# Kernel tuning notes

Measured on AMD Instinct MI355X. Metric: run time of the kernel, lower is better.

## Reference

```python
import jax, jax.numpy as jnp
import numpy as np

B, L, H = 256, 2048, 64

def _min_gru(x, Wz, bz, Wh, bh):
    # x: [B, L, Din] -> h: [B, L, H] via parallel scan of h_t = (1-z_t)*h_{t-1} + z_t*h~_t, h_0 = 0
    z = jax.nn.sigmoid(jnp.einsum('bli,ih->blh', x, Wz) + bz)
    h_tilde = jnp.einsum('bli,ih->blh', x, Wh) + bh
    a = 1.0 - z
    b = z * h_tilde
    def combine(c1, c2):
        a1, b1 = c1
        a2, b2 = c2
        return a1 * a2, b1 * a2 + b2
    _, h = jax.lax.associative_scan(combine, (a, b), axis=1)
    return h

def _stacked(x, Wz0, bz0, Wh0, bh0, Wz1, bz1, Wh1, bh1, Wo, bo):
    h = _min_gru(x, Wz0, bz0, Wh0, bh0)
    h = _min_gru(h, Wz1, bz1, Wh1, bh1)
    return jnp.einsum('blh,ho->blo', h, Wo) + bo  # [B, L, 1]

def setup_inputs():
    key = jax.random.key(0)
    ks = jax.random.split(key, 32)
    inputs = jax.random.bernoulli(ks[0], 0.5, (B, L)).astype(jnp.float32)
    p_array = jax.random.permutation(ks[1], L).astype(jnp.int32)
    def lin(k, fin, fout):
        return (jax.random.normal(k, (fin, fout), jnp.float32) / np.float32(np.sqrt(fin)))
    d = {'inputs': inputs, 'p_array': p_array}
    i = 2
    for r in (1, 2):
        for nm, fin, fout in (('z0', 1, H), ('h0', 1, H), ('z1', H, H), ('h1', H, H), ('o', H, 1)):
            d['w%d%s' % (r, nm)] = lin(ks[i], fin, fout); i += 1
            d['b%d%s' % (r, nm)] = jnp.zeros((fout,), jnp.float32)
    return d

def reference(inputs, p_array, w1z0, b1z0, w1h0, b1h0, w1z1, b1z1, w1h1, b1h1, w1o, b1o,
              w2z0, b2z0, w2h0, b2h0, w2z1, b2z1, w2h1, b2h1, w2o, b2o):
    x = inputs[..., None]                      # [B, L, 1]
    x_sys = _stacked(x, w1z0, b1z0, w1h0, b1h0, w1z1, b1z1, w1h1, b1h1, w1o, b1o)
    x_int = x[:, p_array, :]                   # interleave along sequence dim
    x_p1 = _stacked(x_int, w2z0, b2z0, w2h0, b2h0, w2z1, b2z1, w2h1, b2h1, w2o, b2o)
    x_tx = jnp.concatenate([x_sys, x_p1], axis=2)  # [B, L, 2]
    mean = jnp.mean(x_tx)
    std = jnp.std(x_tx, ddof=1)                # torch.std is unbiased by default
    return (x_tx - mean) / std                 # squeeze(dim=2) is a no-op on size-2 dim
```

## Files before the change

kernel.cpp:

```cpp
#include <hip/hip_runtime.h>

#define BB 256
#define LL 2048
#define HH 64
#define TT 64
#define SS 68
#define NCH (LL / TT)
#define NTOT (BB * LL * 2)

typedef __attribute__((ext_vector_type(8))) short bf16x8;
typedef __attribute__((ext_vector_type(4))) float f32x4;

__device__ __forceinline__ float rcp_(float x)  { return __builtin_amdgcn_rcpf(x); }

__device__ __forceinline__ short f2bf_rne(float f) {
    union { float f; unsigned u; } v; v.f = f;
    unsigned r = v.u + 0x7fff + ((v.u >> 16) & 1);
    return (short)(r >> 16);
}

__device__ __forceinline__ unsigned perm_hi16(float f_hi, float f_lo) {
    union { float f; unsigned u; } a, b;
    a.f = f_hi; b.f = f_lo;
    return __builtin_amdgcn_perm(a.u, b.u, 0x07060302u);
}

template<int D>
__device__ __forceinline__ float rshr(float x) {
    union { float f; int i; } u, r;
    u.f = x;
    r.i = __builtin_amdgcn_update_dpp(0, u.i, 0x110 | D, 0xF, 0xF, true);
    return r.f;
}

__device__ __forceinline__ float bcast7(float x) {
    union { float f; int i; } u, r;
    u.f = x;
    r.i = __builtin_amdgcn_ds_swizzle(u.i, 0x00F8);
    return r.f;
}

__device__ __forceinline__ void p1_scan(const unsigned* __restrict__ bw, int c,
                                        float a0v, float b0v, float a1v, float b1v,
                                        int seg, int col0,
                                        float& carry, float* sh)
{
    const unsigned bits = (bw[c * 2 + (seg >> 2)] >> ((seg & 3) << 3)) & 0xffu;
    float A = 1.0f, Bv = 0.0f;
    #pragma unroll
    for (int i = 0; i < 8; ++i) {
        const bool on = (bits >> i) & 1u;
        const float a = on ? a1v : a0v;
        const float b = on ? b1v : b0v;
        A  = A * a;
        Bv = fmaf(Bv, a, b);
    }
    {
        const float Au = rshr<1>(A), Bu = rshr<1>(Bv);
        if (seg >= 1) { const float Ac = A; A = Au * Ac; Bv = fmaf(Bu, Ac, Bv); }
    }
    {
        const float Au = rshr<2>(A), Bu = rshr<2>(Bv);
        if (seg >= 2) { const float Ac = A; A = Au * Ac; Bv = fmaf(Bu, Ac, Bv); }
    }
    {
        const float Au = rshr<4>(A), Bu = rshr<4>(Bv);
        if (seg >= 4) { const float Ac = A; A = Au * Ac; Bv = fmaf(Bu, Ac, Bv); }
    }
    float Ae = rshr<1>(A), Be = rshr<1>(Bv);
    if (seg == 0) { Ae = 1.0f; Be = 0.0f; }
    float cc = fmaf(Ae, carry, Be);
    #pragma unroll
    for (int i = 0; i < 8; ++i) {
        const bool on = (bits >> i) & 1u;
        const float a = on ? a1v : a0v;
        const float b = on ? b1v : b0v;
        cc = fmaf(a, cc, b);
        sh[(seg * 8 + i) * SS + col0] = cc;
    }
    carry = bcast7(cc);
}

__global__ void __launch_bounds__(512)
__attribute__((amdgpu_waves_per_eu(4, 4)))
gru_fused(const float* __restrict__ x, const int* __restrict__ p,
               const float* __restrict__ w1z0, const float* __restrict__ b1z0,
               const float* __restrict__ w1h0, const float* __restrict__ b1h0,
               const float* __restrict__ w1z1, const float* __restrict__ b1z1,
               const float* __restrict__ w1h1, const float* __restrict__ b1h1,
               const float* __restrict__ w1o,  const float* __restrict__ b1o,
               const float* __restrict__ w2z0, const float* __restrict__ b2z0,
               const float* __restrict__ w2h0, const float* __restrict__ b2h0,
               const float* __restrict__ w2z1, const float* __restrict__ b2z1,
               const float* __restrict__ w2h1, const float* __restrict__ b2h1,
               const float* __restrict__ w2o,  const float* __restrict__ b2o,
               float* __restrict__ out, float* __restrict__ ws)
{
    const int  b  = blockIdx.x;
    const bool pm = (blockIdx.y != 0);

    const float* wz0 = pm ? w2z0 : w1z0;
    const float* bz0 = pm ? b2z0 : b1z0;
    const float* wh0 = pm ? w2h0 : w1h0;
    const float* bh0 = pm ? b2h0 : b1h0;
    const float* wz1 = pm ? w2z1 : w1z1;
    const float* bz1 = pm ? b2z1 : b1z1;
    const float* wh1 = pm ? w2h1 : w1h1;
    const float* bh1 = pm ? b2h1 : b1h1;
    const float* wo  = pm ? w2o  : w1o;
    const float* bov = pm ? b2o  : b1o;

    const int tid   = threadIdx.x;
    const int lane  = tid & 63;
    const int tg    = tid >> 6;
    const int tgu   = __builtin_amdgcn_readfirstlane(tg);
    const int twu   = tgu & 3;
    const int hwu   = tgu >> 2;
    const int q     = lane >> 4;
    const int n     = lane & 15;
    const int seg   = lane & 7;
    const int hidx  = (tgu << 3) | (lane >> 3);

    __shared__ __align__(16) float s_h[2 * TT * SS];
    __shared__ unsigned long long s_xb[LL / 64];
    __shared__ float2 s_w[2][2][4][32];
    __shared__ float s_o[2][4][16];
    __shared__ float s_red[16];

    const float* xrow = x + (size_t)b * LL;

    #pragma unroll
    for (int g = 0; g < 4; ++g) {
        const int idx = g * 512 + tid;
        const int src = pm ? p[idx] : idx;
        const unsigned long long m = __ballot(xrow[src] != 0.0f);
        if (lane == 0) s_xb[g * 8 + tgu] = m;
    }
    const unsigned* bw = (const unsigned*)s_xb;

    const float z0v = rcp_(1.0f + __expf(-bz0[hidx]));
    const float z1v = rcp_(1.0f + __expf(-(wz0[hidx] + bz0[hidx])));
    const float a0v = 1.0f - z0v, b0v = z0v * bh0[hidx];
    const float a1v = 1.0f - z1v, b1v = z1v * (wh0[hidx] + bh0[hidx]);

    float rbz1[2], rbh1[2], rwo4[2];
    #pragma unroll
    for (int ht = 0; ht < 2; ++ht) {
        const int h = hwu * 32 + ht * 16 + n;
        rbz1[ht] = bz1[h];
        rbh1[ht] = bh1[h];
        rwo4[ht] = wo[h];
    }
    const float bo = bov[0];

    bf16x8 wfz[2][2], wfh[2][2];
    for (int ks = 0; ks < 2; ++ks) {
        for (int ht = 0; ht < 2; ++ht) {
            #pragma unroll
            for (int j = 0; j < 8; ++j) {
                const int kk = ks * 32 + q * 8 + j;
                const int h  = hwu * 32 + ht * 16 + n;
                wfz[ks][ht][j] = f2bf_rne(wz1[kk * HH + h]);
                wfh[ks][ht][j] = f2bf_rne(wh1[kk * HH + h]);
            }
        }
    }

    float carry0 = 0.0f;
    float carry1[2] = {0.0f, 0.0f};
    f32x4 ga[2], gb[2];
    float Aqe[2], Bqe[2];
    float pvo[4] = {0, 0, 0, 0};
    float lsum = 0.0f, lsum2 = 0.0f;
    float* outp = out + (pm ? 1 : 0);
    const int t0 = twu * 16;
    const int col0 = hidx ^ (seg << 2);
    const int sswz = (twu * 2 + (n >> 3)) << 2;

    auto g2_step = [&](int cm) {
        if (cm > 0 && hwu == 0 && n == 15) {
            #pragma unroll
            for (int r = 0; r < 4; ++r) {
                const float v = pvo[r] + s_o[(cm - 1) & 1][twu][q * 4 + r] + bo;
                outp[((size_t)b * LL + (cm - 1) * TT + t0 + q * 4 + r) * 2] = v;
                lsum += v;
                lsum2 = fmaf(v, v, lsum2);
            }
        }
        const int buf = cm & 1;
        float Acm[2] = {1, 1}, Bcm[2] = {0, 0};
        float Ap[2], Bp[2];
        #pragma unroll
        for (int w = 0; w < 4; ++w) {
            #pragma unroll
            for (int ht = 0; ht < 2; ++ht) {
                if (w == twu) { Ap[ht] = Acm[ht]; Bp[ht] = Bcm[ht]; }
                const float2 ab = s_w[buf][hwu][w][ht * 16 + n];
                Bcm[ht] = fmaf(ab.x, Bcm[ht], ab.y);
                Acm[ht] *= ab.x;
            }
        }
        float vo[4] = {0, 0, 0, 0};
        #pragma unroll
        for (int ht = 0; ht < 2; ++ht) {
            float cc = fmaf(Aqe[ht], fmaf(Ap[ht], carry1[ht], Bp[ht]), Bqe[ht]);
            #pragma unroll
            for (int r = 0; r < 4; ++r) {
                cc = fmaf(ga[ht][r], cc, gb[ht][r]);
                vo[r] = fmaf(cc, rwo4[ht], vo[r]);
            }
            carry1[ht] = fmaf(Acm[ht], carry1[ht], Bcm[ht]);
        }
        #pragma unroll
        for (int r = 0; r < 4; ++r) {
            vo[r] += rshr<1>(vo[r]);
            vo[r] += rshr<2>(vo[r]);
            vo[r] += rshr<4>(vo[r]);
            vo[r] += rshr<8>(vo[r]);
        }
        if (n == 15) {
            if (hwu) {
                #pragma unroll
                for (int r = 0; r < 4; ++r) s_o[buf][twu][q * 4 + r] = vo[r];
            } else {
                #pragma unroll
                for (int r = 0; r < 4; ++r) pvo[r] = vo[r];
            }
        }
    };

    __syncthreads();

    p1_scan(bw, 0, a0v, b0v, a1v, b1v, seg, col0, carry0, s_h);
    __syncthreads();

    for (int c = 0; c < NCH; ++c) {
        const int cp1 = c + 1;

        if (c > 0) g2_step(c - 1);

        {
            #pragma unroll
            for (int ht = 0; ht < 2; ++ht) {
                ga[ht] = (f32x4){rbz1[ht], rbz1[ht], rbz1[ht], rbz1[ht]};
                gb[ht] = (f32x4){rbh1[ht], rbh1[ht], rbh1[ht], rbh1[ht]};
            }
            const float* shR = s_h + (c & 1) * (TT * SS);
            #pragma unroll
            for (int ks = 0; ks < 2; ++ks) {
                const int base = ks * 32 + q * 8;
                const float* rowp = &shR[(t0 + n) * SS];
                const float4 av0 = *(const float4*)(rowp + (base ^ sswz));
                const float4 av1 = *(const float4*)(rowp + ((base + 4) ^ sswz));
                float af[8] = {av0.x, av0.y, av0.z, av0.w, av1.x, av1.y, av1.z, av1.w};
                union { bf16x8 v; unsigned d[4]; } ahi, alo;
                float rem[8];
                #pragma unroll
                for (int j = 0; j < 8; ++j) {
                    union { float f; unsigned u; } uf; uf.f = af[j];
                    union { unsigned u; float f; } hf; hf.u = uf.u & 0xffff0000u;
                    rem[j] = af[j] - hf.f;
                }
                #pragma unroll
                for (int k = 0; k < 4; ++k) {
                    ahi.d[k] = perm_hi16(af[2 * k + 1], af[2 * k]);
                    alo.d[k] = perm_hi16(rem[2 * k + 1], rem[2 * k]);
                }
                #pragma unroll
                for (int ht = 0; ht < 2; ++ht) {
                    ga[ht] = __builtin_amdgcn_mfma_f32_16x16x32_bf16(ahi.v, wfz[ks][ht], ga[ht], 0, 0, 0);
                    ga[ht] = __builtin_amdgcn_mfma_f32_16x16x32_bf16(alo.v, wfz[ks][ht], ga[ht], 0, 0, 0);
                    gb[ht] = __builtin_amdgcn_mfma_f32_16x16x32_bf16(ahi.v, wfh[ks][ht], gb[ht], 0, 0, 0);
                    gb[ht] = __builtin_amdgcn_mfma_f32_16x16x32_bf16(alo.v, wfh[ks][ht], gb[ht], 0, 0, 0);
                }
            }
            #pragma unroll
            for (int ht = 0; ht < 2; ++ht) {
                #pragma unroll
                for (int r = 0; r < 4; ++r) {
                    const float v   = ga[ht][r];
                    const float a   = rcp_(1.0f + __expf(v));
                    const float htl = gb[ht][r];
                    ga[ht][r] = a;
                    gb[ht][r] = fmaf(-a, htl, htl);
                }
            }
            float Aq[2], Bq[2];
            #pragma unroll
            for (int ht = 0; ht < 2; ++ht) {
                float A = 1.0f, B = 0.0f;
                #pragma unroll
                for (int r = 0; r < 4; ++r) {
                    B = fmaf(ga[ht][r], B, gb[ht][r]);
                    A = A * ga[ht][r];
                }
                Aq[ht] = A; Bq[ht] = B;
            }
            #pragma unroll
            for (int ht = 0; ht < 2; ++ht) {
                const float Au = __shfl_up(Aq[ht], 16), Bu = __shfl_up(Bq[ht], 16);
                if (q >= 1) { const float Ac = Aq[ht]; Aq[ht] = Ac * Au; Bq[ht] = fmaf(Ac, Bu, Bq[ht]); }
            }
            #pragma unroll
            for (int ht = 0; ht < 2; ++ht) {
                const float Au = __shfl_up(Aq[ht], 32), Bu = __shfl_up(Bq[ht], 32);
                if (q >= 2) { const float Ac = Aq[ht]; Aq[ht] = Ac * Au; Bq[ht] = fmaf(Ac, Bu, Bq[ht]); }
            }
            #pragma unroll
            for (int ht = 0; ht < 2; ++ht) {
                const float Ae = __shfl_up(Aq[ht], 16), Be = __shfl_up(Bq[ht], 16);
                Aqe[ht] = (q == 0) ? 1.0f : Ae;
                Bqe[ht] = (q == 0) ? 0.0f : Be;
            }
            if (q == 3) {
                #pragma unroll
                for (int ht = 0; ht < 2; ++ht)
                    s_w[c & 1][hwu][twu][ht * 16 + n] = make_float2(Aq[ht], Bq[ht]);
            }
        }

        if (cp1 < NCH)
            p1_scan(bw, cp1, a0v, b0v, a1v, b1v, seg, col0, carry0,
                    s_h + (cp1 & 1) * (TT * SS));

        __syncthreads();
    }

    g2_step(NCH - 1);
    __syncthreads();
    if (hwu == 0 && n == 15) {
        #pragma unroll
        for (int r = 0; r < 4; ++r) {
            const float v = pvo[r] + s_o[(NCH - 1) & 1][twu][q * 4 + r] + bo;
            outp[((size_t)b * LL + (NCH - 1) * TT + t0 + q * 4 + r) * 2] = v;
            lsum += v;
            lsum2 = fmaf(v, v, lsum2);
        }
    }

    #pragma unroll
    for (int o = 32; o; o >>= 1) {
        lsum  += __shfl_down(lsum, o);
        lsum2 += __shfl_down(lsum2, o);
    }
    if (lane == 0) { s_red[tgu] = lsum; s_red[8 + tgu] = lsum2; }
    __syncthreads();
    if (tid == 0) {
        float s = 0.0f, s2 = 0.0f;
        #pragma unroll
        for (int i = 0; i < 8; ++i) { s += s_red[i]; s2 += s_red[8 + i]; }
        const int gb2 = b * 2 + (pm ? 1 : 0);
        ws[2 * gb2]     = s;
        ws[2 * gb2 + 1] = s2;
    }
}

__global__ void normalize_k(float* __restrict__ out, const float* __restrict__ ws)
{
    __shared__ float s_red[8];
    float s = 0.0f, s2 = 0.0f;
    for (int i = threadIdx.x; i < 2 * BB; i += 256) {
        s  += ws[2 * i];
        s2 += ws[2 * i + 1];
    }
    #pragma unroll
    for (int o = 32; o; o >>= 1) {
        s  += __shfl_down(s, o);
        s2 += __shfl_down(s2, o);
    }
    const int wid = threadIdx.x >> 6;
    if ((threadIdx.x & 63) == 0) { s_red[wid] = s; s_red[4 + wid] = s2; }
    __syncthreads();
    const float tot  = s_red[0] + s_red[1] + s_red[2] + s_red[3];
    const float tot2 = s_red[4] + s_red[5] + s_red[6] + s_red[7];
    const float N    = (float)NTOT;
    const float mean = tot / N;
    const float var  = (tot2 - N * mean * mean) / (N - 1.0f);
    const float inv  = rsqrtf(var);

    const int i = blockIdx.x * blockDim.x + threadIdx.x;
    float4* o4 = (float4*)out;
    float4 v = o4[i];
    v.x = (v.x - mean) * inv;
    v.y = (v.y - mean) * inv;
    v.z = (v.z - mean) * inv;
    v.w = (v.w - mean) * inv;
    o4[i] = v;
}

extern "C" void kernel_launch(void* const* d_in, const int* in_sizes, int n_in,
                              void* d_out, int out_size, void* d_ws, size_t ws_size,
                              hipStream_t stream)
{
    (void)in_sizes; (void)n_in; (void)out_size; (void)ws_size;
    const float* x = (const float*)d_in[0];
    const int*   p = (const int*)d_in[1];
    float* out = (float*)d_out;
    float* ws  = (float*)d_ws;

    dim3 grid(BB, 2);
    gru_fused<<<grid, 512, 0, stream>>>(
        x, p,
        (const float*)d_in[2],  (const float*)d_in[3],
        (const float*)d_in[4],  (const float*)d_in[5],
        (const float*)d_in[6],  (const float*)d_in[7],
        (const float*)d_in[8],  (const float*)d_in[9],
        (const float*)d_in[10], (const float*)d_in[11],
        (const float*)d_in[12], (const float*)d_in[13],
        (const float*)d_in[14], (const float*)d_in[15],
        (const float*)d_in[16], (const float*)d_in[17],
        (const float*)d_in[18], (const float*)d_in[19],
        (const float*)d_in[20], (const float*)d_in[21],
        out, ws);

    normalize_k<<<NTOT / 4 / 256, 256, 0, stream>>>(out, ws);
}
```

Measured before the change: 185.5 us.

## Double threads per block and store layer-1 states pre-split into bf16 hi/lo

```diff
diff --git a/kernel.cpp b/kernel.cpp
--- a/kernel.cpp
+++ b/kernel.cpp
@@ -4,7 +4,7 @@
 #define LL 2048
 #define HH 64
 #define TT 64
-#define SS 68
+#define SH 72
 #define NCH (LL / TT)
 #define NTOT (BB * LL * 2)
 
@@ -17,12 +17,6 @@
     union { float f; unsigned u; } v; v.f = f;
     unsigned r = v.u + 0x7fff + ((v.u >> 16) & 1);
     return (short)(r >> 16);
-}
-
-__device__ __forceinline__ unsigned perm_hi16(float f_hi, float f_lo) {
-    union { float f; unsigned u; } a, b;
-    a.f = f_hi; b.f = f_lo;
-    return __builtin_amdgcn_perm(a.u, b.u, 0x07060302u);
 }
 
 template<int D>
@@ -33,27 +27,27 @@
     return r.f;
 }
 
-__device__ __forceinline__ float bcast7(float x) {
+__device__ __forceinline__ float bcast15(float x) {
     union { float f; int i; } u, r;
     u.f = x;
-    r.i = __builtin_amdgcn_ds_swizzle(u.i, 0x00F8);
+    r.i = __builtin_amdgcn_ds_swizzle(u.i, 0x01F0);
     return r.f;
 }
 
 __device__ __forceinline__ void p1_scan(const unsigned* __restrict__ bw, int c,
                                         float a0v, float b0v, float a1v, float b1v,
-                                        int seg, int col0,
-                                        float& carry, float* sh)
+                                        int seg, int pos0,
+                                        float& carry, short* shh, short* shl)
 {
-    const unsigned bits = (bw[c * 2 + (seg >> 2)] >> ((seg & 3) << 3)) & 0xffu;
+    const unsigned bits = (bw[c * 2 + (seg >> 3)] >> ((seg & 7) << 2)) & 0xFu;
     float A = 1.0f, Bv = 0.0f;
     #pragma unroll
-    for (int i = 0; i < 8; ++i) {
+    for (int i = 0; i < 4; ++i) {
         const bool on = (bits >> i) & 1u;
         const float a = on ? a1v : a0v;
-        const float b = on ? b1v : b0v;
+        const float bb = on ? b1v : b0v;
         A  = A * a;
-        Bv = fmaf(Bv, a, b);
+        Bv = fmaf(Bv, a, bb);
     }
     {
         const float Au = rshr<1>(A), Bu = rshr<1>(Bv);
@@ -67,22 +61,31 @@
         const float Au = rshr<4>(A), Bu = rshr<4>(Bv);
         if (seg >= 4) { const float Ac = A; A = Au * Ac; Bv = fmaf(Bu, Ac, Bv); }
     }
+    {
+        const float Au = rshr<8>(A), Bu = rshr<8>(Bv);
+        if (seg >= 8) { const float Ac = A; A = Au * Ac; Bv = fmaf(Bu, Ac, Bv); }
+    }
     float Ae = rshr<1>(A), Be = rshr<1>(Bv);
     if (seg == 0) { Ae = 1.0f; Be = 0.0f; }
     float cc = fmaf(Ae, carry, Be);
     #pragma unroll
-    for (int i = 0; i < 8; ++i) {
+    for (int i = 0; i < 4; ++i) {
         const bool on = (bits >> i) & 1u;
         const float a = on ? a1v : a0v;
-        const float b = on ? b1v : b0v;
-        cc = fmaf(a, cc, b);
-        sh[(seg * 8 + i) * SS + col0] = cc;
-    }
-    carry = bcast7(cc);
-}
-
-__global__ void __launch_bounds__(512)
-__attribute__((amdgpu_waves_per_eu(4, 4)))
+        const float bb = on ? b1v : b0v;
+        cc = fmaf(a, cc, bb);
+        const int row = seg * 4 + i;
+        union { float f; unsigned u; } uf; uf.f = cc;
+        shh[row * SH + pos0] = (short)(uf.u >> 16);
+        union { unsigned u; float f; } hf; hf.u = uf.u & 0xffff0000u;
+        union { float f; unsigned u; } ur; ur.f = cc - hf.f;
+        shl[row * SH + pos0] = (short)(ur.u >> 16);
+    }
+    carry = bcast15(cc);
+}
+
+__global__ void __launch_bounds__(1024)
+__attribute__((amdgpu_waves_per_eu(8, 8)))
 gru_fused(const float* __restrict__ x, const int* __restrict__ p,
                const float* __restrict__ w1z0, const float* __restrict__ b1z0,
                const float* __restrict__ w1h0, const float* __restrict__ b1h0,
@@ -118,23 +121,24 @@
     const int hwu   = tgu >> 2;
     const int q     = lane >> 4;
     const int n     = lane & 15;
-    const int seg   = lane & 7;
-    const int hidx  = (tgu << 3) | (lane >> 3);
-
-    __shared__ __align__(16) float s_h[2 * TT * SS];
+    const int seg   = lane & 15;
+    const int hidx  = (tgu << 2) | (lane >> 4);
+
     __shared__ unsigned long long s_xb[LL / 64];
-    __shared__ float2 s_w[2][2][4][32];
-    __shared__ float s_o[2][4][16];
-    __shared__ float s_red[16];
+    __shared__ __align__(16) short s_hh[2][TT][SH];
+    __shared__ __align__(16) short s_hl[2][TT][SH];
+    __shared__ float2 s_w[2][4][4][16];
+    __shared__ float  s_o[2][3][4][16];
+    __shared__ float  s_red[32];
 
     const float* xrow = x + (size_t)b * LL;
 
     #pragma unroll
-    for (int g = 0; g < 4; ++g) {
-        const int idx = g * 512 + tid;
+    for (int g = 0; g < 2; ++g) {
+        const int idx = g * 1024 + tid;
         const int src = pm ? p[idx] : idx;
         const unsigned long long m = __ballot(xrow[src] != 0.0f);
-        if (lane == 0) s_xb[g * 8 + tgu] = m;
+        if (lane == 0) s_xb[g * 16 + tgu] = m;
     }
     const unsigned* bw = (const unsigned*)s_xb;
 
@@ -143,73 +147,65 @@
     const float a0v = 1.0f - z0v, b0v = z0v * bh0[hidx];
     const float a1v = 1.0f - z1v, b1v = z1v * (wh0[hidx] + bh0[hidx]);
 
-    float rbz1[2], rbh1[2], rwo4[2];
-    #pragma unroll
-    for (int ht = 0; ht < 2; ++ht) {
-        const int h = hwu * 32 + ht * 16 + n;
-        rbz1[ht] = bz1[h];
-        rbh1[ht] = bh1[h];
-        rwo4[ht] = wo[h];
-    }
-    const float bo = bov[0];
-
-    bf16x8 wfz[2][2], wfh[2][2];
+    const int hq = hwu * 16 + n;
+    const float rbz1 = bz1[hq];
+    const float rbh1 = bh1[hq];
+    const float rwo  = wo[hq];
+    const float bo   = bov[0];
+
+    bf16x8 wfz[2], wfh[2];
     for (int ks = 0; ks < 2; ++ks) {
-        for (int ht = 0; ht < 2; ++ht) {
-            #pragma unroll
-            for (int j = 0; j < 8; ++j) {
-                const int kk = ks * 32 + q * 8 + j;
-                const int h  = hwu * 32 + ht * 16 + n;
-                wfz[ks][ht][j] = f2bf_rne(wz1[kk * HH + h]);
-                wfh[ks][ht][j] = f2bf_rne(wh1[kk * HH + h]);
-            }
+        #pragma unroll
+        for (int j = 0; j < 8; ++j) {
+            const int kk = ks * 32 + q * 8 + j;
+            wfz[ks][j] = f2bf_rne(wz1[kk * HH + hq]);
+            wfh[ks][j] = f2bf_rne(wh1[kk * HH + hq]);
         }
     }
 
     float carry0 = 0.0f;
-    float carry1[2] = {0.0f, 0.0f};
-    f32x4 ga[2], gb[2];
-    float Aqe[2], Bqe[2];
+    float carry1 = 0.0f;
+    f32x4 ga, gb;
+    float Aqe, Bqe;
     float pvo[4] = {0, 0, 0, 0};
     float lsum = 0.0f, lsum2 = 0.0f;
     float* outp = out + (pm ? 1 : 0);
     const int t0 = twu * 16;
-    const int col0 = hidx ^ (seg << 2);
-    const int sswz = (twu * 2 + (n >> 3)) << 2;
+    const int pos0 = hidx ^ ((seg & 7) << 3);
+    const int sw   = ((twu * 4 + (n >> 2)) & 7) << 3;
 
     auto g2_step = [&](int cm) {
         if (cm > 0 && hwu == 0 && n == 15) {
+            const int pb = (cm - 1) & 1;
             #pragma unroll
             for (int r = 0; r < 4; ++r) {
-                const float v = pvo[r] + s_o[(cm - 1) & 1][twu][q * 4 + r] + bo;
+                const float v = pvo[r] + s_o[pb][0][twu][q * 4 + r]
+                                       + s_o[pb][1][twu][q * 4 + r]
+                                       + s_o[pb][2][twu][q * 4 + r] + bo;
                 outp[((size_t)b * LL + (cm - 1) * TT + t0 + q * 4 + r) * 2] = v;
                 lsum += v;
                 lsum2 = fmaf(v, v, lsum2);
             }
         }
         const int buf = cm & 1;
-        float Acm[2] = {1, 1}, Bcm[2] = {0, 0};
-        float Ap[2], Bp[2];
+        float Acm = 1.0f, Bcm = 0.0f;
+        float Ap = 1.0f, Bp = 0.0f;
         #pragma unroll
         for (int w = 0; w < 4; ++w) {
-            #pragma unroll
-            for (int ht = 0; ht < 2; ++ht) {
-                if (w == twu) { Ap[ht] = Acm[ht]; Bp[ht] = Bcm[ht]; }
-                const float2 ab = s_w[buf][hwu][w][ht * 16 + n];
-                Bcm[ht] = fmaf(ab.x, Bcm[ht], ab.y);
-                Acm[ht] *= ab.x;
-            }
-        }
-        float vo[4] = {0, 0, 0, 0};
-        #pragma unroll
-        for (int ht = 0; ht < 2; ++ht) {
-            float cc = fmaf(Aqe[ht], fmaf(Ap[ht], carry1[ht], Bp[ht]), Bqe[ht]);
+            if (w == twu) { Ap = Acm; Bp = Bcm; }
+            const float2 ab = s_w[buf][hwu][w][n];
+            Bcm = fmaf(ab.x, Bcm, ab.y);
+            Acm *= ab.x;
+        }
+        float vo[4];
+        {
+            float cc = fmaf(Aqe, fmaf(Ap, carry1, Bp), Bqe);
             #pragma unroll
             for (int r = 0; r < 4; ++r) {
-                cc = fmaf(ga[ht][r], cc, gb[ht][r]);
-                vo[r] = fmaf(cc, rwo4[ht], vo[r]);
-            }
-            carry1[ht] = fmaf(Acm[ht], carry1[ht], Bcm[ht]);
+                cc = fmaf(ga[r], cc, gb[r]);
+                vo[r] = cc * rwo;
+            }
+            carry1 = fmaf(Acm, carry1, Bcm);
         }
         #pragma unroll
         for (int r = 0; r < 4; ++r) {
@@ -221,7 +217,7 @@
         if (n == 15) {
             if (hwu) {
                 #pragma unroll
-                for (int r = 0; r < 4; ++r) s_o[buf][twu][q * 4 + r] = vo[r];
+                for (int r = 0; r < 4; ++r) s_o[buf][hwu - 1][twu][q * 4 + r] = vo[r];
             } else {
                 #pragma unroll
                 for (int r = 0; r < 4; ++r) pvo[r] = vo[r];
@@ -231,7 +227,8 @@
 
     __syncthreads();
 
-    p1_scan(bw, 0, a0v, b0v, a1v, b1v, seg, col0, carry0, s_h);
+    p1_scan(bw, 0, a0v, b0v, a1v, b1v, seg, pos0, carry0,
+            &s_hh[0][0][0], &s_hl[0][0][0]);
     __syncthreads();
 
     for (int c = 0; c < NCH; ++c) {
@@ -240,88 +237,54 @@
         if (c > 0) g2_step(c - 1);
 
         {
-            #pragma unroll
-            for (int ht = 0; ht < 2; ++ht) {
-                ga[ht] = (f32x4){rbz1[ht], rbz1[ht], rbz1[ht], rbz1[ht]};
-                gb[ht] = (f32x4){rbh1[ht], rbh1[ht], rbh1[ht], rbh1[ht]};
-            }
-            const float* shR = s_h + (c & 1) * (TT * SS);
+            ga = (f32x4){rbz1, rbz1, rbz1, rbz1};
+            gb = (f32x4){rbh1, rbh1, rbh1, rbh1};
+            const int buf = c & 1;
+            const short* rh = &s_hh[buf][t0 + n][0];
+            const short* rl = &s_hl[buf][t0 + n][0];
             #pragma unroll
             for (int ks = 0; ks < 2; ++ks) {
-                const int base = ks * 32 + q * 8;
-                const float* rowp = &shR[(t0 + n) * SS];
-                const float4 av0 = *(const float4*)(rowp + (base ^ sswz));
-                const float4 av1 = *(const float4*)(rowp + ((base + 4) ^ sswz));
-                float af[8] = {av0.x, av0.y, av0.z, av0.w, av1.x, av1.y, av1.z, av1.w};
-                union { bf16x8 v; unsigned d[4]; } ahi, alo;
-                float rem[8];
-                #pragma unroll
-                for (int j = 0; j < 8; ++j) {
-                    union { float f; unsigned u; } uf; uf.f = af[j];
-                    union { unsigned u; float f; } hf; hf.u = uf.u & 0xffff0000u;
-                    rem[j] = af[j] - hf.f;
-                }
-                #pragma unroll
-                for (int k = 0; k < 4; ++k) {
-                    ahi.d[k] = perm_hi16(af[2 * k + 1], af[2 * k]);
-                    alo.d[k] = perm_hi16(rem[2 * k + 1], rem[2 * k]);
-                }
-                #pragma unroll
-                for (int ht = 0; ht < 2; ++ht) {
-                    ga[ht] = __builtin_amdgcn_mfma_f32_16x16x32_bf16(ahi.v, wfz[ks][ht], ga[ht], 0, 0, 0);
-                    ga[ht] = __builtin_amdgcn_mfma_f32_16x16x32_bf16(alo.v, wfz[ks][ht], ga[ht], 0, 0, 0);
-                    gb[ht] = __builtin_amdgcn_mfma_f32_16x16x32_bf16(ahi.v, wfh[ks][ht], gb[ht], 0, 0, 0);
-                    gb[ht] = __builtin_amdgcn_mfma_f32_16x16x32_bf16(alo.v, wfh[ks][ht], gb[ht], 0, 0, 0);
-                }
-            }
-            #pragma unroll
-            for (int ht = 0; ht < 2; ++ht) {
-                #pragma unroll
-                for (int r = 0; r < 4; ++r) {
-                    const float v   = ga[ht][r];
-                    const float a   = rcp_(1.0f + __expf(v));
-                    const float htl = gb[ht][r];
-                    ga[ht][r] = a;
-                    gb[ht][r] = fmaf(-a, htl, htl);
-                }
-            }
-            float Aq[2], Bq[2];
-            #pragma unroll
-            for (int ht = 0; ht < 2; ++ht) {
-                float A = 1.0f, B = 0.0f;
-                #pragma unroll
-                for (int r = 0; r < 4; ++r) {
-                    B = fmaf(ga[ht][r], B, gb[ht][r]);
-                    A = A * ga[ht][r];
-                }
-                Aq[ht] = A; Bq[ht] = B;
-            }
-            #pragma unroll
-            for (int ht = 0; ht < 2; ++ht) {
-                const float Au = __shfl_up(Aq[ht], 16), Bu = __shfl_up(Bq[ht], 16);
-                if (q >= 1) { const float Ac = Aq[ht]; Aq[ht] = Ac * Au; Bq[ht] = fmaf(Ac, Bu, Bq[ht]); }
-            }
-            #pragma unroll
-            for (int ht = 0; ht < 2; ++ht) {
-                const float Au = __shfl_up(Aq[ht], 32), Bu = __shfl_up(Bq[ht], 32);
-                if (q >= 2) { const float Ac = Aq[ht]; Aq[ht] = Ac * Au; Bq[ht] = fmaf(Ac, Bu, Bq[ht]); }
-            }
-            #pragma unroll
-            for (int ht = 0; ht < 2; ++ht) {
-                const float Ae = __shfl_up(Aq[ht], 16), Be = __shfl_up(Bq[ht], 16);
-                Aqe[ht] = (q == 0) ? 1.0f : Ae;
-                Bqe[ht] = (q == 0) ? 0.0f : Be;
-            }
-            if (q == 3) {
-                #pragma unroll
-                for (int ht = 0; ht < 2; ++ht)
-                    s_w[c & 1][hwu][twu][ht * 16 + n] = make_float2(Aq[ht], Bq[ht]);
-            }
+                const int pos = (ks * 32 + q * 8) ^ sw;
+                const bf16x8 ahi = *(const bf16x8*)(rh + pos);
+                const bf16x8 alo = *(const bf16x8*)(rl + pos);
+                ga = __builtin_amdgcn_mfma_f32_16x16x32_bf16(ahi, wfz[ks], ga, 0, 0, 0);
+                ga = __builtin_amdgcn_mfma_f32_16x16x32_bf16(alo, wfz[ks], ga, 0, 0, 0);
+                gb = __builtin_amdgcn_mfma_f32_16x16x32_bf16(ahi, wfh[ks], gb, 0, 0, 0);
+                gb = __builtin_amdgcn_mfma_f32_16x16x32_bf16(alo, wfh[ks], gb, 0, 0, 0);
+            }
+            #pragma unroll
+            for (int r = 0; r < 4; ++r) {
+                const float v   = ga[r];
+                const float a   = rcp_(1.0f + __expf(v));
+                const float htl = gb[r];
+                ga[r] = a;
+                gb[r] = fmaf(-a, htl, htl);
+            }
+            float Aq = 1.0f, Bq = 0.0f;
+            #pragma unroll
+            for (int r = 0; r < 4; ++r) {
+                Bq = fmaf(ga[r], Bq, gb[r]);
+                Aq = Aq * ga[r];
+            }
+            {
+                const float Au = __shfl_up(Aq, 16), Bu = __shfl_up(Bq, 16);
+                if (q >= 1) { const float Ac = Aq; Aq = Ac * Au; Bq = fmaf(Ac, Bu, Bq); }
+            }
+            {
+                const float Au = __shfl_up(Aq, 32), Bu = __shfl_up(Bq, 32);
+                if (q >= 2) { const float Ac = Aq; Aq = Ac * Au; Bq = fmaf(Ac, Bu, Bq); }
+            }
+            {
+                const float Ae = __shfl_up(Aq, 16), Be = __shfl_up(Bq, 16);
+                Aqe = (q == 0) ? 1.0f : Ae;
+                Bqe = (q == 0) ? 0.0f : Be;
+            }
+            if (q == 3) s_w[buf][hwu][twu][n] = make_float2(Aq, Bq);
         }
 
         if (cp1 < NCH)
-            p1_scan(bw, cp1, a0v, b0v, a1v, b1v, seg, col0, carry0,
-                    s_h + (cp1 & 1) * (TT * SS));
+            p1_scan(bw, cp1, a0v, b0v, a1v, b1v, seg, pos0, carry0,
+                    &s_hh[cp1 & 1][0][0], &s_hl[cp1 & 1][0][0]);
 
         __syncthreads();
     }
@@ -329,9 +292,12 @@
     g2_step(NCH - 1);
     __syncthreads();
     if (hwu == 0 && n == 15) {
+        const int pb = (NCH - 1) & 1;
         #pragma unroll
         for (int r = 0; r < 4; ++r) {
-            const float v = pvo[r] + s_o[(NCH - 1) & 1][twu][q * 4 + r] + bo;
+            const float v = pvo[r] + s_o[pb][0][twu][q * 4 + r]
+                                   + s_o[pb][1][twu][q * 4 + r]
+                                   + s_o[pb][2][twu][q * 4 + r] + bo;
             outp[((size_t)b * LL + (NCH - 1) * TT + t0 + q * 4 + r) * 2] = v;
             lsum += v;
             lsum2 = fmaf(v, v, lsum2);
@@ -343,12 +309,12 @@
         lsum  += __shfl_down(lsum, o);
         lsum2 += __shfl_down(lsum2, o);
     }
-    if (lane == 0) { s_red[tgu] = lsum; s_red[8 + tgu] = lsum2; }
+    if (lane == 0) { s_red[tgu] = lsum; s_red[16 + tgu] = lsum2; }
     __syncthreads();
     if (tid == 0) {
         float s = 0.0f, s2 = 0.0f;
         #pragma unroll
-        for (int i = 0; i < 8; ++i) { s += s_red[i]; s2 += s_red[8 + i]; }
+        for (int i = 0; i < 16; ++i) { s += s_red[i]; s2 += s_red[16 + i]; }
         const int gb2 = b * 2 + (pm ? 1 : 0);
         ws[2 * gb2]     = s;
         ws[2 * gb2 + 1] = s2;
@@ -399,7 +365,7 @@
     float* ws  = (float*)d_ws;
 
     dim3 grid(BB, 2);
-    gru_fused<<<grid, 512, 0, stream>>>(
+    gru_fused<<<grid, 1024, 0, stream>>>(
         x, p,
         (const float*)d_in[2],  (const float*)d_in[3],
         (const float*)d_in[4],  (const float*)d_in[5],
```

New measurement: 269.8 us. +45.5%, slower.
